# Kernel tuning notes

Measured on AMD Instinct MI355X. Metric: run time of the kernel, lower is better.

Reference implementation:

```python
import jax, jax.numpy as jnp
import numpy as np

N_NODES = 50000
N_EDGES = 800000
NFEAT = 256
NHID = 128
LATENT = 64


def setup_inputs() -> dict:
    key = jax.random.key(0)
    ks = jax.random.split(key, 8)
    x = jax.random.normal(ks[0], (N_NODES, NFEAT), dtype=jnp.float32)
    src = jax.random.randint(ks[1], (N_EDGES,), 0, N_NODES, dtype=jnp.int32)
    dst = jax.random.randint(ks[2], (N_EDGES,), 0, N_NODES, dtype=jnp.int32)
    edge_weight = jax.random.uniform(ks[3], (N_EDGES,), dtype=jnp.float32)
    W1 = jax.random.normal(ks[4], (NFEAT, NHID), dtype=jnp.float32) / np.sqrt(NFEAT)
    b1 = jnp.zeros((NHID,), dtype=jnp.float32)
    Wmu = jax.random.normal(ks[5], (NHID, LATENT), dtype=jnp.float32) / np.sqrt(NHID)
    bmu = jnp.zeros((LATENT,), dtype=jnp.float32)
    Wlv = jax.random.normal(ks[6], (NHID, LATENT), dtype=jnp.float32) / np.sqrt(NHID)
    blv = jnp.zeros((LATENT,), dtype=jnp.float32)
    return {"x": x, "src": src, "dst": dst, "edge_weight": edge_weight,
            "W1": W1, "b1": b1, "Wmu": Wmu, "bmu": bmu, "Wlv": Wlv, "blv": blv}


def gcn_conv(x, W, b, src, dst, edge_weight, n_nodes):
    # GCNConv: linear transform then sparse (weighted) adjacency aggregation.
    h = x @ W                                   # [N, out]
    msg = h[src] * edge_weight[:, None]         # [E, out] gather + scale
    agg = jax.ops.segment_sum(msg, dst, num_segments=n_nodes)  # scatter-add
    return agg + b


def reference(x, src, dst, edge_weight, W1, b1, Wmu, bmu, Wlv, blv):
    h = jax.nn.relu(gcn_conv(x, W1, b1, src, dst, edge_weight, N_NODES))
    mu = gcn_conv(h, Wmu, bmu, src, dst, edge_weight, N_NODES)
    logvar = gcn_conv(h, Wlv, blv, src, dst, edge_weight, N_NODES)
    return (mu, logvar)
```

## Files before the change

kernel.cpp:

```cpp
#include <hip/hip_runtime.h>
#include <hip/hip_bf16.h>

#define N_NODES 50000
#define N_EDGES 800000
#define NFEAT 256
#define NHID 128
#define LATENT 64
#define NB 98
#define BSH 9
#define CT 4096
#define CBLK 196
#define CAP 8960

typedef __attribute__((ext_vector_type(8))) short bf16x8;
typedef __attribute__((ext_vector_type(4))) float f32x4;
typedef __attribute__((ext_vector_type(8))) short short8v;
typedef __attribute__((ext_vector_type(8))) unsigned short ushort8v;

__device__ inline unsigned short f2bf(float f) {
  union { float f; unsigned u; } c; c.f = f;
  unsigned r = (c.u + 0x7FFFu + ((c.u >> 16) & 1u)) >> 16;
  return (unsigned short)r;
}
__device__ inline float bf2f(unsigned short u) {
  union { unsigned u; float f; } c; c.u = ((unsigned)u) << 16;
  return c.f;
}

__launch_bounds__(256)
__global__ void prep_w_kernel(const float* __restrict__ W1,
                              const float* __restrict__ Wmu,
                              const float* __restrict__ Wlv,
                              unsigned short* __restrict__ W1T,
                              unsigned short* __restrict__ WcT,
                              int* __restrict__ bcur) {
  int b = blockIdx.x;
  int t = threadIdx.x;
  if (b < 128) {
    W1T[b * NFEAT + t] = f2bf(W1[(size_t)t * NHID + b]);
  } else if (b < 256) {
    int n = b - 128;
    if (t < NHID) {
      float v = (n < 64) ? Wmu[(size_t)t * LATENT + n]
                         : Wlv[(size_t)t * LATENT + (n - 64)];
      WcT[n * NHID + t] = f2bf(v);
    }
  } else {
    if (t < 128) bcur[t] = 0;
  }
}

__launch_bounds__(256)
__global__ void gemm1_kernel(const float* __restrict__ X,
                             const unsigned short* __restrict__ W1T,
                             unsigned short* __restrict__ XWb) {
  __shared__ short A_lds[64][40];
  const int t = threadIdx.x;
  const int lane = t & 63;
  const int wave = t >> 6;
  const int row0 = blockIdx.x * 64;
  const int l15 = lane & 15, quad = lane >> 4;
  const int srow = t >> 2, skg = t & 3;

  f32x4 acc[4][2];
#pragma unroll
  for (int i = 0; i < 4; i++)
#pragma unroll
    for (int j = 0; j < 2; j++) acc[i][j] = (f32x4){0.f, 0.f, 0.f, 0.f};

  for (int k0 = 0; k0 < NFEAT; k0 += 32) {
    int gr = row0 + srow;
    float4 v0, v1;
    if (gr < N_NODES) {
      const float* p = X + (size_t)gr * NFEAT + k0 + skg * 8;
      v0 = *(const float4*)p;
      v1 = *(const float4*)(p + 4);
    } else {
      v0 = make_float4(0.f, 0.f, 0.f, 0.f);
      v1 = v0;
    }
    short8v s;
    s[0] = f2bf(v0.x); s[1] = f2bf(v0.y); s[2] = f2bf(v0.z); s[3] = f2bf(v0.w);
    s[4] = f2bf(v1.x); s[5] = f2bf(v1.y); s[6] = f2bf(v1.z); s[7] = f2bf(v1.w);
    __syncthreads();
    *(short8v*)&A_lds[srow][skg * 8] = s;
    __syncthreads();

    bf16x8 a[4], b[2];
#pragma unroll
    for (int mt = 0; mt < 4; mt++)
      a[mt] = *(const bf16x8*)&A_lds[mt * 16 + l15][quad * 8];
#pragma unroll
    for (int nt = 0; nt < 2; nt++) {
      int n = wave * 32 + nt * 16 + l15;
      b[nt] = *(const bf16x8*)(W1T + (size_t)n * NFEAT + k0 + quad * 8);
    }
#pragma unroll
    for (int mt = 0; mt < 4; mt++)
#pragma unroll
      for (int nt = 0; nt < 2; nt++)
        acc[mt][nt] = __builtin_amdgcn_mfma_f32_16x16x32_bf16(a[mt], b[nt], acc[mt][nt], 0, 0, 0);
  }
#pragma unroll
  for (int mt = 0; mt < 4; mt++) {
#pragma unroll
    for (int reg = 0; reg < 4; reg++) {
      int gr = row0 + mt * 16 + quad * 4 + reg;
      if (gr < N_NODES) {
#pragma unroll
        for (int nt = 0; nt < 2; nt++) {
          int gc = wave * 32 + nt * 16 + l15;
          XWb[(size_t)gr * NHID + gc] = f2bf(acc[mt][nt][reg]);
        }
      }
    }
  }
}

__launch_bounds__(512)
__global__ void coarse_part_kernel(const int* __restrict__ src,
                                   const int* __restrict__ dst,
                                   const float* __restrict__ ew,
                                   int* __restrict__ bcur,
                                   int2* __restrict__ part) {
  __shared__ int hist[NB], start[NB], cur[NB], gbase[NB];
  __shared__ int sc[128];
  __shared__ int2 stage[CT];
  int t = threadIdx.x;
  if (t < NB) hist[t] = 0;
  __syncthreads();
  int base = blockIdx.x * CT;
#pragma unroll
  for (int k = 0; k < 8; k++) {
    int e = base + t + k * 512;
    if (e < N_EDGES) atomicAdd(&hist[dst[e] >> BSH], 1);
  }
  __syncthreads();
  int v = (t < NB) ? hist[t] : 0;
  if (t < 128) sc[t] = v;
  __syncthreads();
  int x = v;
  for (int ofs = 1; ofs < 128; ofs <<= 1) {
    int y = (t >= ofs && t < 128) ? sc[t - ofs] : 0;
    __syncthreads();
    if (t < 128) { x += y; sc[t] = x; }
    __syncthreads();
  }
  if (t < NB) {
    int st = x - v;
    start[t] = st;
    cur[t] = st;
    gbase[t] = atomicAdd(&bcur[t], hist[t]);
  }
  __syncthreads();
#pragma unroll
  for (int k = 0; k < 8; k++) {
    int e = base + t + k * 512;
    if (e < N_EDGES) {
      int d = dst[e];
      int b = d >> BSH;
      int lp = atomicAdd(&cur[b], 1);
      stage[lp] = make_int2((src[e] << 16) | d, __float_as_int(ew[e]));
    }
  }
  __syncthreads();
  int nedge = min(CT, N_EDGES - base);
  for (int i = t; i < nedge; i += 512) {
    int2 e = stage[i];
    int b = (e.x & 0xffff) >> BSH;
    part[(size_t)b * CAP + gbase[b] + (i - start[b])] = e;
  }
}

__launch_bounds__(512)
__global__ void fine_kernel(const int* __restrict__ bcur,
                            const int2* __restrict__ part,
                            int2* __restrict__ offs,
                            unsigned int* __restrict__ edata) {
  __shared__ int nh[512];
  __shared__ int sc[512];
  int t = threadIdx.x;
  int b = blockIdx.x;
  int base = b * CAP;
  int cnt = bcur[b];
  int nb = b << BSH;
  nh[t] = 0;
  __syncthreads();
  for (int i = t; i < cnt; i += 512) {
    int d = part[base + i].x & 0xffff;
    atomicAdd(&nh[d - nb], 1);
  }
  __syncthreads();
  int v = nh[t];
  sc[t] = v;
  __syncthreads();
  int x = v;
  for (int ofs = 1; ofs < 512; ofs <<= 1) {
    int y = (t >= ofs) ? sc[t - ofs] : 0;
    __syncthreads();
    x += y;
    sc[t] = x;
    __syncthreads();
  }
  int beg = base + (x - v);
  offs[nb + t] = make_int2(beg, beg + v);
  nh[t] = beg;
  __syncthreads();
  for (int i = t; i < cnt; i += 512) {
    int2 e = part[base + i];
    int d = e.x & 0xffff;
    int pos = atomicAdd(&nh[d - nb], 1);
    edata[pos] = (unsigned)(e.x & 0xffff0000) | (unsigned)f2bf(__int_as_float(e.y));
  }
}

__launch_bounds__(512)
__global__ void g1gemm2_kernel(const unsigned short* __restrict__ XWb,
                               const int2* __restrict__ offs,
                               const unsigned int* __restrict__ edata,
                               const float* __restrict__ b1,
                               const unsigned short* __restrict__ WcT,
                               unsigned short* __restrict__ Tb) {
  __shared__ short A_lds[64][136];
  const int t = threadIdx.x;
  const int lane = t & 63;
  const int wave = t >> 6;
  const int row0 = blockIdx.x * 64;
  const int l15 = lane & 15, quad = lane >> 4;

  float bb[8];
#pragma unroll
  for (int k = 0; k < 8; k++) bb[k] = b1[l15 * 8 + k];

  for (int rr = 0; rr < 4; rr++) {
    int rA = wave * 8 + rr;
    int rB = rA + 4;
    int gA = row0 + rA, gB = row0 + rB;
    float accA[8], accB[8];
#pragma unroll
    for (int k = 0; k < 8; k++) { accA[k] = 0.f; accB[k] = 0.f; }
    int jA = 0, eA = 0, jB = 0, eB = 0;
    if (gA < N_NODES) { int2 o = offs[gA]; jA = o.x + quad; eA = o.y; }
    if (gB < N_NODES) { int2 o = offs[gB]; jB = o.x + quad; eB = o.y; }
    while (jA + 4 < eA && jB + 4 < eB) {
      unsigned a0 = edata[jA], a1 = edata[jA + 4];
      unsigned b0 = edata[jB], b1e = edata[jB + 4];
      ushort8v ra0 = *(const ushort8v*)(XWb + (size_t)(a0 >> 16) * NHID + l15 * 8);
      ushort8v ra1 = *(const ushort8v*)(XWb + (size_t)(a1 >> 16) * NHID + l15 * 8);
      ushort8v rb0 = *(const ushort8v*)(XWb + (size_t)(b0 >> 16) * NHID + l15 * 8);
      ushort8v rb1 = *(const ushort8v*)(XWb + (size_t)(b1e >> 16) * NHID + l15 * 8);
      float wa0 = bf2f((unsigned short)(a0 & 0xffffu));
      float wa1 = bf2f((unsigned short)(a1 & 0xffffu));
      float wb0 = bf2f((unsigned short)(b0 & 0xffffu));
      float wb1 = bf2f((unsigned short)(b1e & 0xffffu));
#pragma unroll
      for (int k = 0; k < 8; k++) accA[k] += bf2f(ra0[k]) * wa0;
#pragma unroll
      for (int k = 0; k < 8; k++) accA[k] += bf2f(ra1[k]) * wa1;
#pragma unroll
      for (int k = 0; k < 8; k++) accB[k] += bf2f(rb0[k]) * wb0;
#pragma unroll
      for (int k = 0; k < 8; k++) accB[k] += bf2f(rb1[k]) * wb1;
      jA += 8; jB += 8;
    }
    for (; jA + 4 < eA; jA += 8) {
      unsigned a0 = edata[jA], a1 = edata[jA + 4];
      ushort8v ra0 = *(const ushort8v*)(XWb + (size_t)(a0 >> 16) * NHID + l15 * 8);
      ushort8v ra1 = *(const ushort8v*)(XWb + (size_t)(a1 >> 16) * NHID + l15 * 8);
      float wa0 = bf2f((unsigned short)(a0 & 0xffffu));
      float wa1 = bf2f((unsigned short)(a1 & 0xffffu));
#pragma unroll
      for (int k = 0; k < 8; k++) accA[k] += bf2f(ra0[k]) * wa0;
#pragma unroll
      for (int k = 0; k < 8; k++) accA[k] += bf2f(ra1[k]) * wa1;
    }
    if (jA < eA) {
      unsigned a0 = edata[jA];
      ushort8v ra0 = *(const ushort8v*)(XWb + (size_t)(a0 >> 16) * NHID + l15 * 8);
      float wa0 = bf2f((unsigned short)(a0 & 0xffffu));
#pragma unroll
      for (int k = 0; k < 8; k++) accA[k] += bf2f(ra0[k]) * wa0;
    }
    for (; jB + 4 < eB; jB += 8) {
      unsigned b0 = edata[jB], b1e = edata[jB + 4];
      ushort8v rb0 = *(const ushort8v*)(XWb + (size_t)(b0 >> 16) * NHID + l15 * 8);
      ushort8v rb1 = *(const ushort8v*)(XWb + (size_t)(b1e >> 16) * NHID + l15 * 8);
      float wb0 = bf2f((unsigned short)(b0 & 0xffffu));
      float wb1 = bf2f((unsigned short)(b1e & 0xffffu));
#pragma unroll
      for (int k = 0; k < 8; k++) accB[k] += bf2f(rb0[k]) * wb0;
#pragma unroll
      for (int k = 0; k < 8; k++) accB[k] += bf2f(rb1[k]) * wb1;
    }
    if (jB < eB) {
      unsigned b0 = edata[jB];
      ushort8v rb0 = *(const ushort8v*)(XWb + (size_t)(b0 >> 16) * NHID + l15 * 8);
      float wb0 = bf2f((unsigned short)(b0 & 0xffffu));
#pragma unroll
      for (int k = 0; k < 8; k++) accB[k] += bf2f(rb0[k]) * wb0;
    }
#pragma unroll
    for (int k = 0; k < 8; k++) {
      accA[k] += __shfl_down(accA[k], 32, 64);
      accA[k] += __shfl_down(accA[k], 16, 64);
      accB[k] += __shfl_down(accB[k], 32, 64);
      accB[k] += __shfl_down(accB[k], 16, 64);
    }
    if (lane < 16) {
      short8v sA, sB;
#pragma unroll
      for (int k = 0; k < 8; k++) {
        sA[k] = (short)f2bf(fmaxf(accA[k] + bb[k], 0.f));
        sB[k] = (short)f2bf(fmaxf(accB[k] + bb[k], 0.f));
      }
      *(short8v*)&A_lds[rA][l15 * 8] = sA;
      *(short8v*)&A_lds[rB][l15 * 8] = sB;
    }
  }
  __syncthreads();

  f32x4 acc2[4];
#pragma unroll
  for (int i = 0; i < 4; i++) acc2[i] = (f32x4){0.f, 0.f, 0.f, 0.f};

#pragma unroll
  for (int k0 = 0; k0 < NHID; k0 += 32) {
    bf16x8 a[4], b;
#pragma unroll
    for (int mt = 0; mt < 4; mt++)
      a[mt] = *(const bf16x8*)&A_lds[mt * 16 + l15][k0 + quad * 8];
    {
      int n = wave * 16 + l15;
      b = *(const bf16x8*)(WcT + (size_t)n * NHID + k0 + quad * 8);
    }
#pragma unroll
    for (int mt = 0; mt < 4; mt++)
      acc2[mt] = __builtin_amdgcn_mfma_f32_16x16x32_bf16(a[mt], b, acc2[mt], 0, 0, 0);
  }
#pragma unroll
  for (int mt = 0; mt < 4; mt++) {
#pragma unroll
    for (int reg = 0; reg < 4; reg++) {
      int gr = row0 + mt * 16 + quad * 4 + reg;
      if (gr < N_NODES) {
        int gc = wave * 16 + l15;
        Tb[(size_t)gr * NHID + gc] = f2bf(acc2[mt][reg]);
      }
    }
  }
}

__launch_bounds__(256)
__global__ void gather2_kernel(const unsigned short* __restrict__ Tb,
                               const int2* __restrict__ offs,
                               const unsigned int* __restrict__ edata,
                               const float* __restrict__ bmu,
                               const float* __restrict__ blv,
                               float* __restrict__ out) {
  int wv = (int)((blockIdx.x * blockDim.x + threadIdx.x) >> 6);
  int gA = wv * 2, gB = wv * 2 + 1;
  if (gA >= N_NODES) return;
  int lane = threadIdx.x & 63;
  int quad = lane >> 4;
  int c8 = lane & 15;
  float accA[8], accB[8];
#pragma unroll
  for (int k = 0; k < 8; k++) { accA[k] = 0.f; accB[k] = 0.f; }
  int jA = 0, eA = 0, jB = 0, eB = 0;
  { int2 o = offs[gA]; jA = o.x + quad; eA = o.y; }
  if (gB < N_NODES) { int2 o = offs[gB]; jB = o.x + quad; eB = o.y; }
  while (jA + 4 < eA && jB + 4 < eB) {
    unsigned a0 = edata[jA], a1 = edata[jA + 4];
    unsigned b0 = edata[jB], b1e = edata[jB + 4];
    ushort8v ra0 = *(const ushort8v*)(Tb + (size_t)(a0 >> 16) * NHID + c8 * 8);
    ushort8v ra1 = *(const ushort8v*)(Tb + (size_t)(a1 >> 16) * NHID + c8 * 8);
    ushort8v rb0 = *(const ushort8v*)(Tb + (size_t)(b0 >> 16) * NHID + c8 * 8);
    ushort8v rb1 = *(const ushort8v*)(Tb + (size_t)(b1e >> 16) * NHID + c8 * 8);
    float wa0 = bf2f((unsigned short)(a0 & 0xffffu));
    float wa1 = bf2f((unsigned short)(a1 & 0xffffu));
    float wb0 = bf2f((unsigned short)(b0 & 0xffffu));
    float wb1 = bf2f((unsigned short)(b1e & 0xffffu));
#pragma unroll
    for (int k = 0; k < 8; k++) accA[k] += bf2f(ra0[k]) * wa0;
#pragma unroll
    for (int k = 0; k < 8; k++) accA[k] += bf2f(ra1[k]) * wa1;
#pragma unroll
    for (int k = 0; k < 8; k++) accB[k] += bf2f(rb0[k]) * wb0;
#pragma unroll
    for (int k = 0; k < 8; k++) accB[k] += bf2f(rb1[k]) * wb1;
    jA += 8; jB += 8;
  }
  for (; jA + 4 < eA; jA += 8) {
    unsigned a0 = edata[jA], a1 = edata[jA + 4];
    ushort8v ra0 = *(const ushort8v*)(Tb + (size_t)(a0 >> 16) * NHID + c8 * 8);
    ushort8v ra1 = *(const ushort8v*)(Tb + (size_t)(a1 >> 16) * NHID + c8 * 8);
    float wa0 = bf2f((unsigned short)(a0 & 0xffffu));
    float wa1 = bf2f((unsigned short)(a1 & 0xffffu));
#pragma unroll
    for (int k = 0; k < 8; k++) accA[k] += bf2f(ra0[k]) * wa0;
#pragma unroll
    for (int k = 0; k < 8; k++) accA[k] += bf2f(ra1[k]) * wa1;
  }
  if (jA < eA) {
    unsigned a0 = edata[jA];
    ushort8v ra0 = *(const ushort8v*)(Tb + (size_t)(a0 >> 16) * NHID + c8 * 8);
    float wa0 = bf2f((unsigned short)(a0 & 0xffffu));
#pragma unroll
    for (int k = 0; k < 8; k++) accA[k] += bf2f(ra0[k]) * wa0;
  }
  for (; jB + 4 < eB; jB += 8) {
    unsigned b0 = edata[jB], b1e = edata[jB + 4];
    ushort8v rb0 = *(const ushort8v*)(Tb + (size_t)(b0 >> 16) * NHID + c8 * 8);
    ushort8v rb1 = *(const ushort8v*)(Tb + (size_t)(b1e >> 16) * NHID + c8 * 8);
    float wb0 = bf2f((unsigned short)(b0 & 0xffffu));
    float wb1 = bf2f((unsigned short)(b1e & 0xffffu));
#pragma unroll
    for (int k = 0; k < 8; k++) accB[k] += bf2f(rb0[k]) * wb0;
#pragma unroll
    for (int k = 0; k < 8; k++) accB[k] += bf2f(rb1[k]) * wb1;
  }
  if (jB < eB) {
    unsigned b0 = edata[jB];
    ushort8v rb0 = *(const ushort8v*)(Tb + (size_t)(b0 >> 16) * NHID + c8 * 8);
    float wb0 = bf2f((unsigned short)(b0 & 0xffffu));
#pragma unroll
    for (int k = 0; k < 8; k++) accB[k] += bf2f(rb0[k]) * wb0;
  }
#pragma unroll
  for (int k = 0; k < 8; k++) {
    accA[k] += __shfl_down(accA[k], 32, 64);
    accA[k] += __shfl_down(accA[k], 16, 64);
    accB[k] += __shfl_down(accB[k], 32, 64);
    accB[k] += __shfl_down(accB[k], 16, 64);
  }
  if (lane < 8) {
    const float* bp = bmu + c8 * 8;
    float4 b0 = *(const float4*)bp;
    float4 b1v = *(const float4*)(bp + 4);
    float* op = out + (size_t)gA * LATENT + c8 * 8;
    float4 o0, o1;
    o0.x = accA[0] + b0.x; o0.y = accA[1] + b0.y;
    o0.z = accA[2] + b0.z; o0.w = accA[3] + b0.w;
    o1.x = accA[4] + b1v.x; o1.y = accA[5] + b1v.y;
    o1.z = accA[6] + b1v.z; o1.w = accA[7] + b1v.w;
    *(float4*)op = o0;
    *(float4*)(op + 4) = o1;
    if (gB < N_NODES) {
      float* opB = out + (size_t)gB * LATENT + c8 * 8;
      float4 p0, p1;
      p0.x = accB[0] + b0.x; p0.y = accB[1] + b0.y;
      p0.z = accB[2] + b0.z; p0.w = accB[3] + b0.w;
      p1.x = accB[4] + b1v.x; p1.y = accB[5] + b1v.y;
      p1.z = accB[6] + b1v.z; p1.w = accB[7] + b1v.w;
      *(float4*)opB = p0;
      *(float4*)(opB + 4) = p1;
    }
  } else if (lane < 16) {
    int c = c8 - 8;
    const float* bp = blv + c * 8;
    float4 b0 = *(const float4*)bp;
    float4 b1v = *(const float4*)(bp + 4);
    float* op = out + (size_t)N_NODES * LATENT + (size_t)gA * LATENT + c * 8;
    float4 o0, o1;
    o0.x = accA[0] + b0.x; o0.y = accA[1] + b0.y;
    o0.z = accA[2] + b0.z; o0.w = accA[3] + b0.w;
    o1.x = accA[4] + b1v.x; o1.y = accA[5] + b1v.y;
    o1.z = accA[6] + b1v.z; o1.w = accA[7] + b1v.w;
    *(float4*)op = o0;
    *(float4*)(op + 4) = o1;
    if (gB < N_NODES) {
      float* opB = out + (size_t)N_NODES * LATENT + (size_t)gB * LATENT + c * 8;
      float4 p0, p1;
      p0.x = accB[0] + b0.x; p0.y = accB[1] + b0.y;
      p0.z = accB[2] + b0.z; p0.w = accB[3] + b0.w;
      p1.x = accB[4] + b1v.x; p1.y = accB[5] + b1v.y;
      p1.z = accB[6] + b1v.z; p1.w = accB[7] + b1v.w;
      *(float4*)opB = p0;
      *(float4*)(opB + 4) = p1;
    }
  }
}

extern "C" void kernel_launch(void* const* d_in, const int* in_sizes, int n_in,
                              void* d_out, int out_size, void* d_ws, size_t ws_size,
                              hipStream_t stream) {
  const float* x   = (const float*)d_in[0];
  const int*   src = (const int*)d_in[1];
  const int*   dst = (const int*)d_in[2];
  const float* ew  = (const float*)d_in[3];
  const float* W1  = (const float*)d_in[4];
  const float* b1  = (const float*)d_in[5];
  const float* Wmu = (const float*)d_in[6];
  const float* bmu = (const float*)d_in[7];
  const float* Wlv = (const float*)d_in[8];
  const float* blv = (const float*)d_in[9];
  float* out = (float*)d_out;

  unsigned short* XWb = (unsigned short*)d_ws;
  unsigned short* Tbb = XWb + (size_t)N_NODES * NHID;
  int2* part = (int2*)(Tbb + (size_t)N_NODES * NHID);
  unsigned int* edata = (unsigned int*)(part + (size_t)NB * CAP);
  int2* offs = (int2*)(edata + (size_t)NB * CAP);
  int* bcur  = (int*)(offs + 50176);
  unsigned short* W1T = (unsigned short*)(bcur + 128);
  unsigned short* WcT = W1T + 128 * NFEAT;

  dim3 blk(256);
  int gemm_grid = (N_NODES + 63) / 64;
  int wave_grid2 = ((N_NODES + 1) / 2 * 64 + 255) / 256;

  prep_w_kernel<<<257, blk, 0, stream>>>(W1, Wmu, Wlv, W1T, WcT, bcur);
  gemm1_kernel<<<gemm_grid, blk, 0, stream>>>(x, W1T, XWb);
  coarse_part_kernel<<<CBLK, dim3(512), 0, stream>>>(src, dst, ew, bcur, part);
  fine_kernel<<<NB, dim3(512), 0, stream>>>(bcur, part, offs, edata);
  g1gemm2_kernel<<<gemm_grid, dim3(512), 0, stream>>>(XWb, offs, edata, b1, WcT, Tbb);
  gather2_kernel<<<wave_grid2, blk, 0, stream>>>(Tbb, offs, edata, bmu, blv, out);
}
```

Measured before the change: 230.1 us.

## Merge gemm1 with edge partitioning into one launch and double bucket count

Fuses the first dense GEMM and the coarse edge-partition pass into a single kernel whose blocks branch by index, so the two independent stages run concurrently and share an LDS union. Bucket count is doubled (256-node buckets), which gives the fine CSR-building kernel twice as many, smaller blocks for more parallelism. The g1gemm2 kernel moves to 256-thread blocks, with each wave handling more rows and two MFMA column tiles. The costs are a heterogeneous block mix, higher LDS for GEMM blocks because of the union, and fewer waves per block in the aggregation stage.

```diff
diff --git a/kernel.cpp b/kernel.cpp
--- a/kernel.cpp
+++ b/kernel.cpp
@@ -6,14 +6,16 @@
 #define NFEAT 256
 #define NHID 128
 #define LATENT 64
-#define NB 98
-#define BSH 9
+#define NB 196
+#define BSH 8
 #define CT 4096
 #define CBLK 196
-#define CAP 8960
+#define CAP 4608
+#define GEMM_GRID 782
 
 typedef __attribute__((ext_vector_type(8))) short bf16x8;
 typedef __attribute__((ext_vector_type(4))) float f32x4;
+typedef __attribute__((ext_vector_type(4))) short short4v;
 typedef __attribute__((ext_vector_type(8))) short short8v;
 typedef __attribute__((ext_vector_type(8))) unsigned short ushort8v;
 
@@ -46,129 +48,119 @@
       WcT[n * NHID + t] = f2bf(v);
     }
   } else {
-    if (t < 128) bcur[t] = 0;
-  }
-}
-
-__launch_bounds__(256)
-__global__ void gemm1_kernel(const float* __restrict__ X,
-                             const unsigned short* __restrict__ W1T,
-                             unsigned short* __restrict__ XWb) {
-  __shared__ short A_lds[64][40];
+    bcur[t] = 0;
+  }
+}
+
+__launch_bounds__(512)
+__global__ void gemm1_coarse_kernel(const float* __restrict__ X,
+                                    const unsigned short* __restrict__ W1T,
+                                    unsigned short* __restrict__ XWb,
+                                    const int* __restrict__ src,
+                                    const int* __restrict__ dst,
+                                    const float* __restrict__ ew,
+                                    int* __restrict__ bcur,
+                                    int2* __restrict__ part) {
+  __shared__ union U {
+    struct { short A[64][40]; } g;
+    struct {
+      int hist[NB], start[NB], cur[NB], gbase[NB];
+      int sc[256];
+      int2 stage[CT];
+    } c;
+  } u;
   const int t = threadIdx.x;
-  const int lane = t & 63;
-  const int wave = t >> 6;
-  const int row0 = blockIdx.x * 64;
-  const int l15 = lane & 15, quad = lane >> 4;
-  const int srow = t >> 2, skg = t & 3;
-
-  f32x4 acc[4][2];
-#pragma unroll
-  for (int i = 0; i < 4; i++)
-#pragma unroll
-    for (int j = 0; j < 2; j++) acc[i][j] = (f32x4){0.f, 0.f, 0.f, 0.f};
-
-  for (int k0 = 0; k0 < NFEAT; k0 += 32) {
-    int gr = row0 + srow;
-    float4 v0, v1;
-    if (gr < N_NODES) {
-      const float* p = X + (size_t)gr * NFEAT + k0 + skg * 8;
-      v0 = *(const float4*)p;
-      v1 = *(const float4*)(p + 4);
-    } else {
-      v0 = make_float4(0.f, 0.f, 0.f, 0.f);
-      v1 = v0;
-    }
-    short8v s;
-    s[0] = f2bf(v0.x); s[1] = f2bf(v0.y); s[2] = f2bf(v0.z); s[3] = f2bf(v0.w);
-    s[4] = f2bf(v1.x); s[5] = f2bf(v1.y); s[6] = f2bf(v1.z); s[7] = f2bf(v1.w);
-    __syncthreads();
-    *(short8v*)&A_lds[srow][skg * 8] = s;
-    __syncthreads();
-
-    bf16x8 a[4], b[2];
-#pragma unroll
-    for (int mt = 0; mt < 4; mt++)
-      a[mt] = *(const bf16x8*)&A_lds[mt * 16 + l15][quad * 8];
-#pragma unroll
-    for (int nt = 0; nt < 2; nt++) {
-      int n = wave * 32 + nt * 16 + l15;
-      b[nt] = *(const bf16x8*)(W1T + (size_t)n * NFEAT + k0 + quad * 8);
-    }
-#pragma unroll
-    for (int mt = 0; mt < 4; mt++)
-#pragma unroll
-      for (int nt = 0; nt < 2; nt++)
-        acc[mt][nt] = __builtin_amdgcn_mfma_f32_16x16x32_bf16(a[mt], b[nt], acc[mt][nt], 0, 0, 0);
-  }
-#pragma unroll
-  for (int mt = 0; mt < 4; mt++) {
-#pragma unroll
-    for (int reg = 0; reg < 4; reg++) {
-      int gr = row0 + mt * 16 + quad * 4 + reg;
-      if (gr < N_NODES) {
-#pragma unroll
-        for (int nt = 0; nt < 2; nt++) {
-          int gc = wave * 32 + nt * 16 + l15;
-          XWb[(size_t)gr * NHID + gc] = f2bf(acc[mt][nt][reg]);
+
+  if (blockIdx.x < GEMM_GRID) {
+    const int lane = t & 63;
+    const int wave = t >> 6;
+    const int row0 = blockIdx.x * 64;
+    const int l15 = lane & 15, quad = lane >> 4;
+    const int srow = t >> 3, skg = t & 7;
+
+    f32x4 acc[4];
+#pragma unroll
+    for (int i = 0; i < 4; i++) acc[i] = (f32x4){0.f, 0.f, 0.f, 0.f};
+
+    for (int k0 = 0; k0 < NFEAT; k0 += 32) {
+      int gr = row0 + srow;
+      float4 v = (gr < N_NODES)
+                     ? *(const float4*)(X + (size_t)gr * NFEAT + k0 + skg * 4)
+                     : make_float4(0.f, 0.f, 0.f, 0.f);
+      short4v s;
+      s.x = f2bf(v.x); s.y = f2bf(v.y); s.z = f2bf(v.z); s.w = f2bf(v.w);
+      __syncthreads();
+      *(short4v*)&u.g.A[srow][skg * 4] = s;
+      __syncthreads();
+
+      bf16x8 a[4], b;
+#pragma unroll
+      for (int mt = 0; mt < 4; mt++)
+        a[mt] = *(const bf16x8*)&u.g.A[mt * 16 + l15][quad * 8];
+      {
+        int n = wave * 16 + l15;
+        b = *(const bf16x8*)(W1T + (size_t)n * NFEAT + k0 + quad * 8);
+      }
+#pragma unroll
+      for (int mt = 0; mt < 4; mt++)
+        acc[mt] = __builtin_amdgcn_mfma_f32_16x16x32_bf16(a[mt], b, acc[mt], 0, 0, 0);
+    }
+#pragma unroll
+    for (int mt = 0; mt < 4; mt++) {
+#pragma unroll
+      for (int reg = 0; reg < 4; reg++) {
+        int gr = row0 + mt * 16 + quad * 4 + reg;
+        if (gr < N_NODES) {
+          int gc = wave * 16 + l15;
+          XWb[(size_t)gr * NHID + gc] = f2bf(acc[mt][reg]);
         }
       }
     }
-  }
-}
-
-__launch_bounds__(512)
-__global__ void coarse_part_kernel(const int* __restrict__ src,
-                                   const int* __restrict__ dst,
-                                   const float* __restrict__ ew,
-                                   int* __restrict__ bcur,
-                                   int2* __restrict__ part) {
-  __shared__ int hist[NB], start[NB], cur[NB], gbase[NB];
-  __shared__ int sc[128];
-  __shared__ int2 stage[CT];
-  int t = threadIdx.x;
-  if (t < NB) hist[t] = 0;
-  __syncthreads();
-  int base = blockIdx.x * CT;
-#pragma unroll
-  for (int k = 0; k < 8; k++) {
-    int e = base + t + k * 512;
-    if (e < N_EDGES) atomicAdd(&hist[dst[e] >> BSH], 1);
-  }
-  __syncthreads();
-  int v = (t < NB) ? hist[t] : 0;
-  if (t < 128) sc[t] = v;
-  __syncthreads();
-  int x = v;
-  for (int ofs = 1; ofs < 128; ofs <<= 1) {
-    int y = (t >= ofs && t < 128) ? sc[t - ofs] : 0;
-    __syncthreads();
-    if (t < 128) { x += y; sc[t] = x; }
-    __syncthreads();
-  }
-  if (t < NB) {
-    int st = x - v;
-    start[t] = st;
-    cur[t] = st;
-    gbase[t] = atomicAdd(&bcur[t], hist[t]);
-  }
-  __syncthreads();
-#pragma unroll
-  for (int k = 0; k < 8; k++) {
-    int e = base + t + k * 512;
-    if (e < N_EDGES) {
-      int d = dst[e];
-      int b = d >> BSH;
-      int lp = atomicAdd(&cur[b], 1);
-      stage[lp] = make_int2((src[e] << 16) | d, __float_as_int(ew[e]));
-    }
-  }
-  __syncthreads();
-  int nedge = min(CT, N_EDGES - base);
-  for (int i = t; i < nedge; i += 512) {
-    int2 e = stage[i];
-    int b = (e.x & 0xffff) >> BSH;
-    part[(size_t)b * CAP + gbase[b] + (i - start[b])] = e;
+  } else {
+    int bid = blockIdx.x - GEMM_GRID;
+    if (t < NB) u.c.hist[t] = 0;
+    __syncthreads();
+    int base = bid * CT;
+#pragma unroll
+    for (int k = 0; k < 8; k++) {
+      int e = base + t + k * 512;
+      if (e < N_EDGES) atomicAdd(&u.c.hist[dst[e] >> BSH], 1);
+    }
+    __syncthreads();
+    int v = (t < NB) ? u.c.hist[t] : 0;
+    if (t < 256) u.c.sc[t] = v;
+    __syncthreads();
+    int x = v;
+    for (int ofs = 1; ofs < 256; ofs <<= 1) {
+      int y = (t >= ofs && t < 256) ? u.c.sc[t - ofs] : 0;
+      __syncthreads();
+      if (t < 256) { x += y; u.c.sc[t] = x; }
+      __syncthreads();
+    }
+    if (t < NB) {
+      int st = x - v;
+      u.c.start[t] = st;
+      u.c.cur[t] = st;
+      u.c.gbase[t] = atomicAdd(&bcur[t], u.c.hist[t]);
+    }
+    __syncthreads();
+#pragma unroll
+    for (int k = 0; k < 8; k++) {
+      int e = base + t + k * 512;
+      if (e < N_EDGES) {
+        int d = dst[e];
+        int b = d >> BSH;
+        int lp = atomicAdd(&u.c.cur[b], 1);
+        u.c.stage[lp] = make_int2((src[e] << 16) | d, __float_as_int(ew[e]));
+      }
+    }
+    __syncthreads();
+    int nedge = min(CT, N_EDGES - base);
+    for (int i = t; i < nedge; i += 512) {
+      int2 e = u.c.stage[i];
+      int b = (e.x & 0xffff) >> BSH;
+      part[(size_t)b * CAP + u.c.gbase[b] + (i - u.c.start[b])] = e;
+    }
   }
 }
 
@@ -177,34 +169,35 @@
                             const int2* __restrict__ part,
                             int2* __restrict__ offs,
                             unsigned int* __restrict__ edata) {
-  __shared__ int nh[512];
-  __shared__ int sc[512];
+  __shared__ int nh[256];
+  __shared__ int sc[256];
   int t = threadIdx.x;
   int b = blockIdx.x;
   int base = b * CAP;
   int cnt = bcur[b];
   int nb = b << BSH;
-  nh[t] = 0;
+  if (t < 256) nh[t] = 0;
   __syncthreads();
   for (int i = t; i < cnt; i += 512) {
     int d = part[base + i].x & 0xffff;
     atomicAdd(&nh[d - nb], 1);
   }
   __syncthreads();
-  int v = nh[t];
-  sc[t] = v;
+  int v = (t < 256) ? nh[t] : 0;
+  if (t < 256) sc[t] = v;
   __syncthreads();
   int x = v;
-  for (int ofs = 1; ofs < 512; ofs <<= 1) {
-    int y = (t >= ofs) ? sc[t - ofs] : 0;
-    __syncthreads();
-    x += y;
-    sc[t] = x;
-    __syncthreads();
-  }
-  int beg = base + (x - v);
-  offs[nb + t] = make_int2(beg, beg + v);
-  nh[t] = beg;
+  for (int ofs = 1; ofs < 256; ofs <<= 1) {
+    int y = (t >= ofs && t < 256) ? sc[t - ofs] : 0;
+    __syncthreads();
+    if (t < 256) { x += y; sc[t] = x; }
+    __syncthreads();
+  }
+  if (t < 256) {
+    int beg = base + (x - v);
+    offs[nb + t] = make_int2(beg, beg + v);
+    nh[t] = beg;
+  }
   __syncthreads();
   for (int i = t; i < cnt; i += 512) {
     int2 e = part[base + i];
@@ -214,7 +207,7 @@
   }
 }
 
-__launch_bounds__(512)
+__launch_bounds__(256)
 __global__ void g1gemm2_kernel(const unsigned short* __restrict__ XWb,
                                const int2* __restrict__ offs,
                                const unsigned int* __restrict__ edata,
@@ -232,9 +225,9 @@
 #pragma unroll
   for (int k = 0; k < 8; k++) bb[k] = b1[l15 * 8 + k];
 
-  for (int rr = 0; rr < 4; rr++) {
-    int rA = wave * 8 + rr;
-    int rB = rA + 4;
+  for (int rr = 0; rr < 8; rr++) {
+    int rA = wave * 16 + rr;
+    int rB = rA + 8;
     int gA = row0 + rA, gB = row0 + rB;
     float accA[8], accB[8];
 #pragma unroll
@@ -319,23 +312,28 @@
   }
   __syncthreads();
 
-  f32x4 acc2[4];
-#pragma unroll
-  for (int i = 0; i < 4; i++) acc2[i] = (f32x4){0.f, 0.f, 0.f, 0.f};
+  f32x4 acc2[4][2];
+#pragma unroll
+  for (int i = 0; i < 4; i++)
+#pragma unroll
+    for (int j = 0; j < 2; j++) acc2[i][j] = (f32x4){0.f, 0.f, 0.f, 0.f};
 
 #pragma unroll
   for (int k0 = 0; k0 < NHID; k0 += 32) {
-    bf16x8 a[4], b;
+    bf16x8 a[4], b[2];
 #pragma unroll
     for (int mt = 0; mt < 4; mt++)
       a[mt] = *(const bf16x8*)&A_lds[mt * 16 + l15][k0 + quad * 8];
-    {
-      int n = wave * 16 + l15;
-      b = *(const bf16x8*)(WcT + (size_t)n * NHID + k0 + quad * 8);
+#pragma unroll
+    for (int nt = 0; nt < 2; nt++) {
+      int n = wave * 32 + nt * 16 + l15;
+      b[nt] = *(const bf16x8*)(WcT + (size_t)n * NHID + k0 + quad * 8);
     }
 #pragma unroll
     for (int mt = 0; mt < 4; mt++)
-      acc2[mt] = __builtin_amdgcn_mfma_f32_16x16x32_bf16(a[mt], b, acc2[mt], 0, 0, 0);
+#pragma unroll
+      for (int nt = 0; nt < 2; nt++)
+        acc2[mt][nt] = __builtin_amdgcn_mfma_f32_16x16x32_bf16(a[mt], b[nt], acc2[mt][nt], 0, 0, 0);
   }
 #pragma unroll
   for (int mt = 0; mt < 4; mt++) {
@@ -343,8 +341,11 @@
     for (int reg = 0; reg < 4; reg++) {
       int gr = row0 + mt * 16 + quad * 4 + reg;
       if (gr < N_NODES) {
-        int gc = wave * 16 + l15;
-        Tb[(size_t)gr * NHID + gc] = f2bf(acc2[mt][reg]);
+#pragma unroll
+        for (int nt = 0; nt < 2; nt++) {
+          int gc = wave * 32 + nt * 16 + l15;
+          Tb[(size_t)gr * NHID + gc] = f2bf(acc2[mt][nt][reg]);
+        }
       }
     }
   }
@@ -502,17 +503,16 @@
   unsigned int* edata = (unsigned int*)(part + (size_t)NB * CAP);
   int2* offs = (int2*)(edata + (size_t)NB * CAP);
   int* bcur  = (int*)(offs + 50176);
-  unsigned short* W1T = (unsigned short*)(bcur + 128);
+  unsigned short* W1T = (unsigned short*)(bcur + 256);
   unsigned short* WcT = W1T + 128 * NFEAT;
 
   dim3 blk(256);
-  int gemm_grid = (N_NODES + 63) / 64;
   int wave_grid2 = ((N_NODES + 1) / 2 * 64 + 255) / 256;
 
   prep_w_kernel<<<257, blk, 0, stream>>>(W1, Wmu, Wlv, W1T, WcT, bcur);
-  gemm1_kernel<<<gemm_grid, blk, 0, stream>>>(x, W1T, XWb);
-  coarse_part_kernel<<<CBLK, dim3(512), 0, stream>>>(src, dst, ew, bcur, part);
+  gemm1_coarse_kernel<<<GEMM_GRID + CBLK, dim3(512), 0, stream>>>(
+      x, W1T, XWb, src, dst, ew, bcur, part);
   fine_kernel<<<NB, dim3(512), 0, stream>>>(bcur, part, offs, edata);
-  g1gemm2_kernel<<<gemm_grid, dim3(512), 0, stream>>>(XWb, offs, edata, b1, WcT, Tbb);
+  g1gemm2_kernel<<<GEMM_GRID, blk, 0, stream>>>(XWb, offs, edata, b1, WcT, Tbb);
   gather2_kernel<<<wave_grid2, blk, 0, stream>>>(Tbb, offs, edata, bmu, blv, out);
 }
```

Result: faster. 212.4 us, median of 2 (-7.7%).
